# Kernel optimization log

Measured on AMD Instinct MI355X. Metric: run time of the kernel, lower is better.

The kernel has to match this reference:

```python
import jax, jax.numpy as jnp
import numpy as np
from functools import partial

B, EMB, H, V, T = 128, 512, 1024, 8192, 100
START_VALUE = 0


def setup_inputs() -> dict:
    key = jax.random.key(0)
    ks = jax.random.split(key, 8)
    s = 0.05
    return {
        "x": jax.random.normal(ks[0], (B, H), jnp.float32),
        "emb_table": jax.random.normal(ks[1], (V, EMB), jnp.float32) * s,
        "w_ih": jax.random.normal(ks[2], (3 * H, EMB), jnp.float32) * s,
        "w_hh": jax.random.normal(ks[3], (3 * H, H), jnp.float32) * s,
        "b_ih": jax.random.normal(ks[4], (3 * H,), jnp.float32) * s,
        "b_hh": jax.random.normal(ks[5], (3 * H,), jnp.float32) * s,
        "cls_w": jax.random.normal(ks[6], (V, H), jnp.float32) * s,
        "cls_b": jax.random.normal(ks[7], (V,), jnp.float32) * s,
    }


def _gru_cell(e, h, w_ih, w_hh, b_ih, b_hh):
    # PyTorch GRU cell math. e: [B,EMB], h: [B,H]
    gi = e @ w_ih.T + b_ih  # [B, 3H]
    gh = h @ w_hh.T + b_hh  # [B, 3H]
    i_r, i_z, i_n = jnp.split(gi, 3, axis=1)
    h_r, h_z, h_n = jnp.split(gh, 3, axis=1)
    r = jax.nn.sigmoid(i_r + h_r)
    z = jax.nn.sigmoid(i_z + h_z)
    n = jnp.tanh(i_n + r * h_n)
    return (1.0 - z) * n + z * h


def reference(x, emb_table, w_ih, w_hh, b_ih, b_hh, cls_w, cls_b):
    # start distribution: log_softmax of one-hot at START_VALUE
    start_val = jax.nn.log_softmax(
        jnp.zeros((V,), x.dtype).at[START_VALUE].set(1.0), axis=0
    )
    prev0 = jnp.broadcast_to(start_val, (B, V))

    def step(carry, _):
        h, prev_logp = carry
        idx = jnp.argmax(prev_logp, axis=1)          # [B]
        e = emb_table[idx]                           # [B, EMB]
        h_new = _gru_cell(e, h, w_ih, w_hh, b_ih, b_hh)
        logp = jax.nn.log_softmax(h_new @ cls_w.T + cls_b, axis=1)  # [B, V]
        return (h_new, logp), logp

    _, outs = jax.lax.scan(step, (x, prev0), None, length=T - 1)
    outs = jnp.transpose(outs, (1, 0, 2))            # [B, T-1, V]
    return jnp.concatenate([prev0[:, None, :], outs], axis=1)  # [B, T, V]
```

## Files before the change

kernel.cpp:

```cpp
#include <hip/hip_runtime.h>
#include <stdint.h>


#define Bb   128
#define EMBd 512
#define Hd   1024
#define Vd   8192
#define Td   100
#define HPB  524288

typedef __attribute__((ext_vector_type(8))) _Float16 half8;
typedef __attribute__((ext_vector_type(4))) float f32x4;
typedef unsigned long long ull;

#define LOSCALE 2048.0f
#define LOINV   (1.0f/2048.0f)

#define WAITV(N) do { asm volatile("s_waitcnt vmcnt(" #N ")" ::: "memory"); \
                      __builtin_amdgcn_sched_barrier(0); } while (0)
#define WAITL    do { asm volatile("s_waitcnt lgkmcnt(0)" ::: "memory");    \
                      __builtin_amdgcn_sched_barrier(0); } while (0)

__device__ __forceinline__ uint32_t fkey(float f) {
  uint32_t u = __float_as_uint(f);
  return (u & 0x80000000u) ? ~u : (u | 0x80000000u);
}
__device__ __forceinline__ ull umax64(ull a, ull b) { return a > b ? a : b; }

__device__ __forceinline__ void dma16(const void* g, void* l) {
  __builtin_amdgcn_global_load_lds((const uint32_t*)g, (uint32_t*)l, 16, 0, 0);
}
__device__ __forceinline__ void st16sc(void* p, half8 v) {
  f32x4 d = *(f32x4*)&v;
  asm volatile("global_store_dwordx4 %0, %1, off sc0 sc1"
               :: "v"(p), "v"(d) : "memory");
}
__device__ __forceinline__ ull sysld64(const ull* p) {
  return __hip_atomic_load((ull*)p, __ATOMIC_RELAXED, __HIP_MEMORY_SCOPE_SYSTEM);
}

__device__ __forceinline__ void cvt8(const float4 v0, const float4 v1,
                                     half8& hh, half8& ll) {
  float vv[8] = {v0.x, v0.y, v0.z, v0.w, v1.x, v1.y, v1.z, v1.w};
#pragma unroll
  for (int i = 0; i < 8; ++i) {
    _Float16 h = (_Float16)vv[i];
    hh[i] = h;
    ll[i] = (_Float16)((vv[i] - (float)h) * LOSCALE);
  }
}

__global__ void k_init(const float* __restrict__ x, float* __restrict__ hbuf0,
                       ull* __restrict__ amax, char* __restrict__ hpre0,
                       uint32_t* __restrict__ bar) {
  int tid = blockIdx.x * 256 + threadIdx.x;
  if (tid < Bb * Hd) hbuf0[tid] = x[tid];
  if (tid < Td * Bb) amax[tid] = (tid < Bb) ? 0xFFFFFFFFull : 0ull;
  if (tid >= 16384 && tid < 16384 + 256) bar[tid - 16384] = 0;
  if (tid < 16384) {
    int b = tid & 127, sc = tid >> 7;
    int st = sc >> 2, c = sc & 3;
    const float* src = x + b * Hd + st * 32 + c * 8;
    float4 v0 = *(const float4*)src, v1 = *(const float4*)(src + 4);
    half8 hh, ll; cvt8(v0, v1, hh, ll);
    char* hp = hpre0 + st * 16384 + b * 128;
    *(half8*)(hp + ((c       ^ (b & 7))) * 16) = hh;
    *(half8*)(hp + (((c + 4) ^ (b & 7))) * 16) = ll;
  }
}

__global__ void k_prep_emb(const float* __restrict__ emb, char* __restrict__ embp) {
  int t = blockIdx.x * 256 + threadIdx.x;
  int row = t >> 6, rem = t & 63, st = rem >> 2, c = rem & 3;
  const float* src = emb + (size_t)row * EMBd + st * 32 + c * 8;
  float4 v0 = *(const float4*)src, v1 = *(const float4*)(src + 4);
  half8 hh, ll; cvt8(v0, v1, hh, ll);
  char* d = embp + (size_t)row * 2048 + st * 128;
  *(half8*)(d + c * 16) = hh;
  *(half8*)(d + (c + 4) * 16) = ll;
}

__global__ void k_prep_w(const float* __restrict__ w_ih, const float* __restrict__ w_hh,
                         char* __restrict__ wpre) {
  int bi = blockIdx.x;
  int st = bi % 12, t2 = bi / 12, q = t2 & 3, cg = t2 >> 2;
  int t = threadIdx.x; if (t >= 192) return;
  int r = t >> 2, c = t & 3;
  int g = r >> 4, bn = r & 15;
  int k0 = q * 384 + st * 32 + c * 8;
  const float* src = (k0 < 512)
    ? (w_ih + (size_t)(g * 1024 + cg * 16 + bn) * EMBd + k0)
    : (w_hh + (size_t)(g * 1024 + cg * 16 + bn) * Hd + (k0 - 512));
  float4 v0 = *(const float4*)src, v1 = *(const float4*)(src + 4);
  half8 hh, ll; cvt8(v0, v1, hh, ll);
  char* d = wpre + (size_t)bi * 6144 + r * 128;
  *(half8*)(d + ((c       ^ (r & 7))) * 16) = hh;
  *(half8*)(d + (((c + 4) ^ (r & 7))) * 16) = ll;
}

__global__ void k_prep_cls(const float* __restrict__ cls_w, char* __restrict__ clsp) {
  int b = blockIdx.x;
  int ct = b >> 5, st = b & 31;
  int t = threadIdx.x;
  int r = t >> 2, c = t & 3;
  const float* src = cls_w + (size_t)(ct * 64 + r) * Hd + st * 32 + c * 8;
  float4 v0 = *(const float4*)src, v1 = *(const float4*)(src + 4);
  half8 hh, ll; cvt8(v0, v1, hh, ll);
  char* d = clsp + (size_t)b * 8192 + r * 128;
  *(half8*)(d + ((c       ^ (r & 7))) * 16) = hh;
  *(half8*)(d + (((c + 4) ^ (r & 7))) * 16) = ll;
}

__global__ __launch_bounds__(256, 2) void k_prep_gi(
    const char* __restrict__ embp, const char* __restrict__ wpre,
    const float* __restrict__ b_ih, float* __restrict__ gi)
{
  const int cg = blockIdx.x, vh = blockIdx.y;
  const int tid = threadIdx.x, lane = tid & 63, w = tid >> 6;
  const int C = cg * 16;
  __shared__ __align__(16) char pA[4 * 8192];
  __shared__ __align__(16) char pB[4 * 6144];

  f32x4 accH[3], accL[3];
#pragma unroll
  for (int g = 0; g < 3; ++g) {
    accH[g] = (f32x4){0.f, 0.f, 0.f, 0.f};
    accL[g] = (f32x4){0.f, 0.f, 0.f, 0.f};
  }

  const int rr = lane >> 3, cc = lane & 7;
  const char* abase = embp + (size_t)(vh * 64 + w * 16 + rr) * 2048 + ((cc ^ rr) * 16);

  auto issue = [&](int st) {
    char* da = pA + (st & 3) * 8192 + w * 2048;
    const char* s0 = abase + st * 128;
    dma16(s0, da);
    dma16(s0 + 8 * 2048, da + 1024);
    const int wq = st / 12, wst = st - wq * 12;
    const char* sb = wpre + (size_t)((cg * 4 + wq) * 12 + wst) * 6144 + w * 1536 + lane * 16;
    char* db = pB + (st & 3) * 6144 + w * 1536;
    dma16(sb, db);
    if (lane < 32) dma16(sb + 1024, db + 1024);
  };

  const int l15 = lane & 15, qd = lane >> 4, r7 = l15 & 7;
  const int offAH = (w * 16 + l15) * 128 + ((qd)     ^ r7) * 16;
  const int offAL = (w * 16 + l15) * 128 + ((qd + 4) ^ r7) * 16;

  issue(0); issue(1); issue(2);
  WAITV(8);
  __builtin_amdgcn_s_barrier();

  for (int st = 0; st < 16; ++st) {
    const int bf = st & 3;
    half8 aH = *(half8*)&pA[bf * 8192 + offAH];
    half8 aL = *(half8*)&pA[bf * 8192 + offAL];
    if (st + 3 < 16) issue(st + 3);
#pragma unroll
    for (int g = 0; g < 3; ++g) {
      half8 bH = *(half8*)&pB[bf * 6144 + (g * 16 + l15) * 128 + ((qd)     ^ r7) * 16];
      half8 bL = *(half8*)&pB[bf * 6144 + (g * 16 + l15) * 128 + ((qd + 4) ^ r7) * 16];
      accH[g] = __builtin_amdgcn_mfma_f32_16x16x32_f16(aH, bH, accH[g], 0, 0, 0);
      accL[g] = __builtin_amdgcn_mfma_f32_16x16x32_f16(aH, bL, accL[g], 0, 0, 0);
      accL[g] = __builtin_amdgcn_mfma_f32_16x16x32_f16(aL, bH, accL[g], 0, 0, 0);
    }
    if (st < 15) {
      if (st <= 12)      { WAITV(8); }
      else if (st == 13) { WAITV(4); }
      else               { WAITV(0); }
      WAITL;
      __builtin_amdgcn_s_barrier();
    }
  }

  const int v0 = vh * 64 + w * 16 + qd * 4;
#pragma unroll
  for (int g = 0; g < 3; ++g) {
    float bi = b_ih[g * 1024 + C + l15];
#pragma unroll
    for (int i = 0; i < 4; ++i) {
      float val = accH[g][i] + accL[g][i] * LOINV + bi;
      gi[(size_t)(v0 + i) * 3072 + g * 1024 + C + l15] = val;
    }
  }
}

__device__ __forceinline__ void relbar(uint32_t* __restrict__ bar, int wg, uint32_t gen) {
  __syncthreads();
  if (threadIdx.x == 0) {
    const int g = wg & 7;
    uint32_t old = __hip_atomic_fetch_add(&bar[g * 16], 1u, __ATOMIC_RELAXED,
                                          __HIP_MEMORY_SCOPE_SYSTEM);
    if (old + 1u == gen * 32u)
      __hip_atomic_fetch_add(&bar[128], 1u, __ATOMIC_RELAXED,
                             __HIP_MEMORY_SCOPE_SYSTEM);
    while (__hip_atomic_load(&bar[128], __ATOMIC_RELAXED,
                             __HIP_MEMORY_SCOPE_SYSTEM) < gen * 8u)
      __builtin_amdgcn_s_sleep(4);
  }
  __syncthreads();
}

__global__ __launch_bounds__(256) void k_loop(
    const char* __restrict__ wpre, const char* __restrict__ clsp,
    const float* __restrict__ gi,
    const float* __restrict__ b_hh, const float* __restrict__ cls_b,
    float* __restrict__ hbuf, char* __restrict__ hpre,
    ull* __restrict__ amax, float* __restrict__ out,
    uint32_t* __restrict__ bar)
{
  const int wg = blockIdx.x;
  const int tid = threadIdx.x, lane = tid & 63, w = tid >> 6;
  __shared__ __align__(16) char smem[81920];

  if (tid == 0)
    (void)__hip_atomic_load(&bar[160], __ATOMIC_ACQUIRE, __HIP_MEMORY_SCOPE_AGENT);
  __syncthreads();

  const int l15 = lane & 15, qd = lane >> 4, r7 = l15 & 7;

  const int cg = wg & 63, rh = (wg >> 6) & 1;
  const int C = cg * 16;
  const int ct = wg & 127, rt0 = wg >> 7;
  const int r0c = rt0 * 64, c0c = ct * 64;
  const char* c_bsrc = clsp + (size_t)ct * 262144 + w * 2048 + lane * 16;

  const int offA_H = (w * 16 + l15) * 128 + ((qd)     ^ r7) * 16;
  const int offA_L = (w * 16 + l15) * 128 + ((qd + 4) ^ r7) * 16;

  uint32_t gen = 0;

  for (int s = 1; s < Td; ++s) {
    const int pPrev = (s - 1) & 1, pCur = s & 1;
    const char* hpre_rd = hpre + (size_t)(s - 1) * HPB;
    char*       hpre_wr = hpre + (size_t)s * HPB;

    if (wg < 128) {
      const ull* amax_prev = amax + (size_t)(s - 1) * Bb;
      const char* hsrc = hpre_rd + rh * 8192 + w * 2048 + lane * 16;
      char* gA = smem;
      char* gB = smem + 32768;

      f32x4 accH[3], accL[3];
#pragma unroll
      for (int g = 0; g < 3; ++g) {
        accH[g] = (f32x4){0.f, 0.f, 0.f, 0.f};
        accL[g] = (f32x4){0.f, 0.f, 0.f, 0.f};
      }

      auto issue = [&](int st) {
        char* da = gA + (st & 3) * 8192 + w * 2048;
        const char* sa = hsrc + st * 16384;
        dma16(sa, da);
        dma16(sa + 1024, da + 1024);
        const int k0 = 512 + st * 32;
        const int wq = (k0 >= 1152) ? 3 : (k0 >= 768 ? 2 : 1);
        const int wst = (k0 - wq * 384) >> 5;
        const char* sb = wpre + (size_t)((cg * 4 + wq) * 12 + wst) * 6144 + w * 1536 + lane * 16;
        char* db = gB + (st & 3) * 6144 + w * 1536;
        dma16(sb, db);
        if (lane < 32) dma16(sb + 1024, db + 1024);
      };

      issue(0); issue(1); issue(2);
      WAITV(8);
      __builtin_amdgcn_s_barrier();

      for (int st = 0; st < 32; ++st) {
        const int bf = st & 3;
        half8 aH = *(half8*)&gA[bf * 8192 + offA_H];
        half8 aL = *(half8*)&gA[bf * 8192 + offA_L];
        if (st + 3 < 32) issue(st + 3);
#pragma unroll
        for (int g = 0; g < 3; ++g) {
          half8 bH = *(half8*)&gB[bf * 6144 + (g * 16 + l15) * 128 + ((qd)     ^ r7) * 16];
          half8 bL = *(half8*)&gB[bf * 6144 + (g * 16 + l15) * 128 + ((qd + 4) ^ r7) * 16];
          accH[g] = __builtin_amdgcn_mfma_f32_16x16x32_f16(aH, bH, accH[g], 0, 0, 0);
          accL[g] = __builtin_amdgcn_mfma_f32_16x16x32_f16(aH, bL, accL[g], 0, 0, 0);
          accL[g] = __builtin_amdgcn_mfma_f32_16x16x32_f16(aL, bH, accL[g], 0, 0, 0);
        }
        if (st < 31) {
          if (st <= 28)      { WAITV(8); }
          else if (st == 29) { WAITV(4); }
          else               { WAITV(0); }
          WAITL;
          __builtin_amdgcn_s_barrier();
        }
      }

      const int j = C + l15;
      const float bh0 = b_hh[j], bh1 = b_hh[1024 + j], bh2 = b_hh[2048 + j];
      const float* hprev_f = hbuf + (size_t)pPrev * Bb * Hd;
      float* hnew_f = hbuf + (size_t)pCur * Bb * Hd;
      float outs[4];
#pragma unroll
      for (int i = 0; i < 4; ++i) {
        const int ri = rh * 64 + w * 16 + qd * 4 + i;
        const uint32_t idx = (~(uint32_t)sysld64(&amax_prev[ri])) & 8191u;
        const float* gp = gi + (size_t)idx * 3072 + j;
        float i_r = gp[0], i_z = gp[1024], i_n = gp[2048];
        float h_r = accH[0][i] + accL[0][i] * LOINV + bh0;
        float h_z = accH[1][i] + accL[1][i] * LOINV + bh1;
        float h_n = accH[2][i] + accL[2][i] * LOINV + bh2;
        float rr2 = 1.f / (1.f + expf(-(i_r + h_r)));
        float zz = 1.f / (1.f + expf(-(i_z + h_z)));
        float nn = tanhf(i_n + rr2 * h_n);
        float o = (1.f - zz) * nn + zz * hprev_f[ri * Hd + j];
        hnew_f[ri * Hd + j] = o;
        outs[i] = o;
      }
      __syncthreads();
      float* sT = (float*)smem;
#pragma unroll
      for (int i = 0; i < 4; ++i)
        sT[(w * 16 + qd * 4 + i) * 16 + l15] = outs[i];
      __syncthreads();
      if (tid < 128) {
        const int row = tid >> 1, half = tid & 1;
        const int b = rh * 64 + row;
        const float* srcp = sT + row * 16 + half * 8;
        half8 hh, ll;
#pragma unroll
        for (int e = 0; e < 8; ++e) {
          float o = srcp[e];
          _Float16 oh = (_Float16)o;
          hh[e] = oh;
          ll[e] = (_Float16)((o - (float)oh) * LOSCALE);
        }
        const int stp = C >> 5;
        const int chb = ((C & 31) >> 3) + half;
        char* hp = hpre_wr + stp * 16384 + b * 128;
        st16sc(hp + ((chb       ^ (b & 7))) * 16, hh);
        st16sc(hp + (((chb + 4) ^ (b & 7))) * 16, ll);
      }
    }

    ++gen; relbar(bar, wg, gen);

    {
      const char* asrc = hpre_wr + rt0 * 8192 + w * 2048 + lane * 16;
      char* cA = smem;
      char* cB = smem + 32768;

      f32x4 accH[4], accL[4];
#pragma unroll
      for (int i = 0; i < 4; ++i) {
        accH[i] = (f32x4){0.f, 0.f, 0.f, 0.f};
        accL[i] = (f32x4){0.f, 0.f, 0.f, 0.f};
      }

      auto issue = [&](int st) {
        char* da = cA + (st & 3) * 8192 + w * 2048;
        const char* sa = asrc + st * 16384;
        dma16(sa, da);
        dma16(sa + 1024, da + 1024);
        char* db = cB + (st & 3) * 8192 + w * 2048;
        const char* sb = c_bsrc + st * 8192;
        dma16(sb, db);
        dma16(sb + 1024, db + 1024);
      };

      issue(0); issue(1); issue(2);
      WAITV(8);
      __builtin_amdgcn_s_barrier();

      for (int st = 0; st < 32; ++st) {
        const int bf = st & 3;
        half8 aH = *(half8*)&cA[bf * 8192 + offA_H];
        half8 aL = *(half8*)&cA[bf * 8192 + offA_L];
        if (st + 3 < 32) issue(st + 3);
#pragma unroll
        for (int cf = 0; cf < 4; ++cf) {
          half8 bH = *(half8*)&cB[bf * 8192 + (cf * 16 + l15) * 128 + ((qd)     ^ r7) * 16];
          half8 bL = *(half8*)&cB[bf * 8192 + (cf * 16 + l15) * 128 + ((qd + 4) ^ r7) * 16];
          accH[cf] = __builtin_amdgcn_mfma_f32_16x16x32_f16(aH, bH, accH[cf], 0, 0, 0);
          accL[cf] = __builtin_amdgcn_mfma_f32_16x16x32_f16(aH, bL, accL[cf], 0, 0, 0);
          accL[cf] = __builtin_amdgcn_mfma_f32_16x16x32_f16(aL, bH, accL[cf], 0, 0, 0);
        }
        if (st < 31) {
          if (st <= 28)      { WAITV(8); }
          else if (st == 29) { WAITV(4); }
          else               { WAITV(0); }
          WAITL;
          __builtin_amdgcn_s_barrier();
        }
      }

      float bsv[4];
#pragma unroll
      for (int cf = 0; cf < 4; ++cf) bsv[cf] = cls_b[c0c + cf * 16 + l15];
#pragma unroll
      for (int i = 0; i < 4; ++i) {
        const int brow = r0c + w * 16 + qd * 4 + i;
        float* orow = out + ((size_t)brow * Td + s) * Vd;
        ull best = 0ull;
#pragma unroll
        for (int cf = 0; cf < 4; ++cf) {
          const int v = c0c + cf * 16 + l15;
          float val = accH[cf][i] + accL[cf][i] * LOINV + bsv[cf];
          __builtin_nontemporal_store(val, &orow[v]);
          best = umax64(best, ((ull)fkey(val) << 32) | (uint32_t)(~(uint32_t)v));
        }
        best = umax64(best, __shfl_xor(best, 1));
        best = umax64(best, __shfl_xor(best, 2));
        best = umax64(best, __shfl_xor(best, 4));
        best = umax64(best, __shfl_xor(best, 8));
        if (l15 == 0) atomicMax(&amax[(size_t)s * Bb + brow], best);
      }
    }

    ++gen; relbar(bar, wg, gen);
  }
}

__global__ void k_softmax(float* __restrict__ out,
                          const ull* __restrict__ amax) {
  int blk = blockIdx.x;
  int t = blk % Td, b = blk / Td;
  int tid = threadIdx.x;
  float* row = out + ((size_t)b * Td + t) * Vd;
  if (t == 0) {
    float lse0 = logf(expf(1.0f) + (float)(Vd - 1));
    for (int i = tid; i < Vd; i += 256) row[i] = ((i == 0) ? 1.0f : 0.0f) - lse0;
    return;
  }
  ull key = amax[t * Bb + b];
  uint32_t ku = (uint32_t)(key >> 32);
  uint32_t u = (ku & 0x80000000u) ? (ku & 0x7fffffffu) : ~ku;
  float m = __uint_as_float(u);
  float x[32];
  float ssum = 0.f;
#pragma unroll
  for (int i = 0; i < 32; ++i) {
    x[i] = row[tid + i * 256];
    ssum += expf(x[i] - m);
  }
  ssum += __shfl_xor(ssum, 1);
  ssum += __shfl_xor(ssum, 2);
  ssum += __shfl_xor(ssum, 4);
  ssum += __shfl_xor(ssum, 8);
  ssum += __shfl_xor(ssum, 16);
  ssum += __shfl_xor(ssum, 32);
  __shared__ float wsum[4];
  if ((tid & 63) == 0) wsum[tid >> 6] = ssum;
  __syncthreads();
  float lse = m + logf(wsum[0] + wsum[1] + wsum[2] + wsum[3]);
#pragma unroll
  for (int i = 0; i < 32; ++i) row[tid + i * 256] = x[i] - lse;
}

extern "C" void kernel_launch(void* const* d_in, const int* in_sizes, int n_in,
                              void* d_out, int out_size, void* d_ws, size_t ws_size,
                              hipStream_t stream) {
  const float* x     = (const float*)d_in[0];
  const float* emb   = (const float*)d_in[1];
  const float* w_ih  = (const float*)d_in[2];
  const float* w_hh  = (const float*)d_in[3];
  const float* b_ih  = (const float*)d_in[4];
  const float* b_hh  = (const float*)d_in[5];
  const float* cls_w = (const float*)d_in[6];
  const float* cls_b = (const float*)d_in[7];
  float* out = (float*)d_out;

  char* ws = (char*)d_ws;
  size_t o = 0;
  ull*      amax = (ull*)(ws + o);      o += (size_t)Td * Bb * 8;
  uint32_t* bar  = (uint32_t*)(ws + o); o += 1024;
  float*    hbuf = (float*)(ws + o);    o += (size_t)2 * Bb * Hd * 4;
  char*     hpre = ws + o;              o += (size_t)Td * HPB;
  char*     embp = ws + o;              o += (size_t)Vd * 2048;
  char*     wpre = ws + o;              o += (size_t)3072 * 6144;
  char*     clsp = ws + o;              o += (size_t)128 * 32 * 8192;
  float*    gi   = (float*)(ws + o);    o += (size_t)Vd * 3072 * 4;

  k_init<<<512, 256, 0, stream>>>(x, hbuf, amax, hpre, bar);
  k_prep_emb<<<2048, 256, 0, stream>>>(emb, embp);
  k_prep_w<<<3072, 256, 0, stream>>>(w_ih, w_hh, wpre);
  k_prep_cls<<<4096, 256, 0, stream>>>(cls_w, clsp);
  k_prep_gi<<<dim3(64, 128), 256, 0, stream>>>(embp, wpre, b_ih, gi);

  k_loop<<<256, 256, 0, stream>>>(wpre, clsp, gi, b_hh, cls_b,
                                  hbuf, hpre, amax, out, bar);

  k_softmax<<<12800, 256, 0, stream>>>(out, amax);
}
```

Measured before the change: 4.325 ms.

## Split GRU and classifier into dedicated workgroups with flag-based producer/consumer sync

Replaces the two global barriers per timestep with per-step readiness counters. The first 128 workgroups do the GRU step and publish an hReady counter. The remaining workgroups compute the classifier, each covering two column tiles, and publish per-step completion counts. The GRU's hidden-state matmul for step s can now overlap the classifier of step s-1, and it waits for the argmax only before the gate update. In exchange, each classifier workgroup does twice the work with a larger LDS footprint, and correctness depends on the grid size and the counter initialization matching.

Measured after the change: 4.366 ms. No clear change (+0.9%).

```diff
diff --git a/kernel.cpp b/kernel.cpp
--- a/kernel.cpp
+++ b/kernel.cpp
@@ -38,6 +38,15 @@
 __device__ __forceinline__ ull sysld64(const ull* p) {
   return __hip_atomic_load((ull*)p, __ATOMIC_RELAXED, __HIP_MEMORY_SCOPE_SYSTEM);
 }
+__device__ __forceinline__ uint32_t ld32sys(uint32_t* p) {
+  return __hip_atomic_load(p, __ATOMIC_RELAXED, __HIP_MEMORY_SCOPE_SYSTEM);
+}
+__device__ __forceinline__ void st32sys(uint32_t* p, uint32_t v) {
+  __hip_atomic_store(p, v, __ATOMIC_RELAXED, __HIP_MEMORY_SCOPE_SYSTEM);
+}
+__device__ __forceinline__ uint32_t add32sys(uint32_t* p, uint32_t v) {
+  return __hip_atomic_fetch_add(p, v, __ATOMIC_RELAXED, __HIP_MEMORY_SCOPE_SYSTEM);
+}
 
 __device__ __forceinline__ void cvt8(const float4 v0, const float4 v1,
                                      half8& hh, half8& ll) {
@@ -56,7 +65,8 @@
   int tid = blockIdx.x * 256 + threadIdx.x;
   if (tid < Bb * Hd) hbuf0[tid] = x[tid];
   if (tid < Td * Bb) amax[tid] = (tid < Bb) ? 0xFFFFFFFFull : 0ull;
-  if (tid >= 16384 && tid < 16384 + 256) bar[tid - 16384] = 0;
+  if (tid >= 16384 && tid < 16640)
+    bar[tid - 16384] = (tid - 16384 == 8) ? 128u : 0u;
   if (tid < 16384) {
     int b = tid & 127, sc = tid >> 7;
     int st = sc >> 2, c = sc & 3;
@@ -185,22 +195,6 @@
   }
 }
 
-__device__ __forceinline__ void relbar(uint32_t* __restrict__ bar, int wg, uint32_t gen) {
-  __syncthreads();
-  if (threadIdx.x == 0) {
-    const int g = wg & 7;
-    uint32_t old = __hip_atomic_fetch_add(&bar[g * 16], 1u, __ATOMIC_RELAXED,
-                                          __HIP_MEMORY_SCOPE_SYSTEM);
-    if (old + 1u == gen * 32u)
-      __hip_atomic_fetch_add(&bar[128], 1u, __ATOMIC_RELAXED,
-                             __HIP_MEMORY_SCOPE_SYSTEM);
-    while (__hip_atomic_load(&bar[128], __ATOMIC_RELAXED,
-                             __HIP_MEMORY_SCOPE_SYSTEM) < gen * 8u)
-      __builtin_amdgcn_s_sleep(4);
-  }
-  __syncthreads();
-}
-
 __global__ __launch_bounds__(256) void k_loop(
     const char* __restrict__ wpre, const char* __restrict__ clsp,
     const float* __restrict__ gi,
@@ -211,35 +205,32 @@
 {
   const int wg = blockIdx.x;
   const int tid = threadIdx.x, lane = tid & 63, w = tid >> 6;
-  __shared__ __align__(16) char smem[81920];
+  __shared__ __align__(16) char smem[98304];
 
   if (tid == 0)
-    (void)__hip_atomic_load(&bar[160], __ATOMIC_ACQUIRE, __HIP_MEMORY_SCOPE_AGENT);
+    (void)__hip_atomic_load(&bar[200], __ATOMIC_ACQUIRE, __HIP_MEMORY_SCOPE_AGENT);
   __syncthreads();
 
+  uint32_t* gCnt   = &bar[0];
+  uint32_t* hReady = &bar[1];
+  uint32_t* aCnt   = &bar[8];
+
   const int l15 = lane & 15, qd = lane >> 4, r7 = l15 & 7;
-
-  const int cg = wg & 63, rh = (wg >> 6) & 1;
-  const int C = cg * 16;
-  const int ct = wg & 127, rt0 = wg >> 7;
-  const int r0c = rt0 * 64, c0c = ct * 64;
-  const char* c_bsrc = clsp + (size_t)ct * 262144 + w * 2048 + lane * 16;
-
   const int offA_H = (w * 16 + l15) * 128 + ((qd)     ^ r7) * 16;
   const int offA_L = (w * 16 + l15) * 128 + ((qd + 4) ^ r7) * 16;
 
-  uint32_t gen = 0;
-
-  for (int s = 1; s < Td; ++s) {
-    const int pPrev = (s - 1) & 1, pCur = s & 1;
-    const char* hpre_rd = hpre + (size_t)(s - 1) * HPB;
-    char*       hpre_wr = hpre + (size_t)s * HPB;
-
-    if (wg < 128) {
-      const ull* amax_prev = amax + (size_t)(s - 1) * Bb;
-      const char* hsrc = hpre_rd + rh * 8192 + w * 2048 + lane * 16;
-      char* gA = smem;
-      char* gB = smem + 32768;
+  if (wg < 128) {
+    const int cg = wg & 63, rh = wg >> 6;
+    const int C = cg * 16;
+    char* gA = smem;
+    char* gB = smem + 32768;
+
+    for (int s = 1; s < Td; ++s) {
+      if (tid == 0)
+        while (ld32sys(hReady) < (uint32_t)(s - 1)) __builtin_amdgcn_s_sleep(2);
+      __syncthreads();
+
+      const char* hsrc = hpre + (size_t)(s - 1) * HPB + rh * 8192 + w * 2048 + lane * 16;
 
       f32x4 accH[3], accL[3];
 #pragma unroll
@@ -288,10 +279,15 @@
         }
       }
 
+      if (tid == 0)
+        while (ld32sys(&aCnt[s - 1]) < 128u) __builtin_amdgcn_s_sleep(2);
+      __syncthreads();
+
       const int j = C + l15;
       const float bh0 = b_hh[j], bh1 = b_hh[1024 + j], bh2 = b_hh[2048 + j];
-      const float* hprev_f = hbuf + (size_t)pPrev * Bb * Hd;
-      float* hnew_f = hbuf + (size_t)pCur * Bb * Hd;
+      const float* hprev_f = hbuf + (size_t)((s - 1) & 1) * Bb * Hd;
+      float* hnew_f = hbuf + (size_t)(s & 1) * Bb * Hd;
+      const ull* amax_prev = amax + (size_t)(s - 1) * Bb;
       float outs[4];
 #pragma unroll
       for (int i = 0; i < 4; ++i) {
@@ -329,22 +325,37 @@
         }
         const int stp = C >> 5;
         const int chb = ((C & 31) >> 3) + half;
-        char* hp = hpre_wr + stp * 16384 + b * 128;
+        char* hp = hpre + (size_t)s * HPB + stp * 16384 + b * 128;
         st16sc(hp + ((chb       ^ (b & 7))) * 16, hh);
         st16sc(hp + (((chb + 4) ^ (b & 7))) * 16, ll);
       }
+      WAITV(0);
+      __syncthreads();
+      if (tid == 0) {
+        uint32_t old = add32sys(gCnt, 1u);
+        if (old + 1u == 128u * (uint32_t)s)
+          st32sys(hReady, (uint32_t)s);
+      }
     }
-
-    ++gen; relbar(bar, wg, gen);
-
-    {
-      const char* asrc = hpre_wr + rt0 * 8192 + w * 2048 + lane * 16;
-      char* cA = smem;
-      char* cB = smem + 32768;
-
-      f32x4 accH[4], accL[4];
-#pragma unroll
-      for (int i = 0; i < 4; ++i) {
+  } else {
+    const int wgC = wg - 128;
+    const int ct2 = wgC & 63, rt0 = wgC >> 6;
+    const int r0c = rt0 * 64;
+    char* cA = smem;
+    char* cB = smem + 32768;
+    const char* bb0 = clsp + (size_t)(2 * ct2)     * 262144 + w * 2048 + lane * 16;
+    const char* bb1 = clsp + (size_t)(2 * ct2 + 1) * 262144 + w * 2048 + lane * 16;
+
+    for (int s = 1; s < Td; ++s) {
+      if (tid == 0)
+        while (ld32sys(hReady) < (uint32_t)s) __builtin_amdgcn_s_sleep(2);
+      __syncthreads();
+
+      const char* asrc = hpre + (size_t)s * HPB + rt0 * 8192 + w * 2048 + lane * 16;
+
+      f32x4 accH[8], accL[8];
+#pragma unroll
+      for (int i = 0; i < 8; ++i) {
         accH[i] = (f32x4){0.f, 0.f, 0.f, 0.f};
         accL[i] = (f32x4){0.f, 0.f, 0.f, 0.f};
       }
@@ -354,14 +365,17 @@
         const char* sa = asrc + st * 16384;
         dma16(sa, da);
         dma16(sa + 1024, da + 1024);
-        char* db = cB + (st & 3) * 8192 + w * 2048;
-        const char* sb = c_bsrc + st * 8192;
-        dma16(sb, db);
-        dma16(sb + 1024, db + 1024);
+        char* db = cB + (st & 3) * 16384 + w * 2048;
+        const char* s0 = bb0 + st * 8192;
+        dma16(s0, db);
+        dma16(s0 + 1024, db + 1024);
+        const char* s1 = bb1 + st * 8192;
+        dma16(s1, db + 8192);
+        dma16(s1 + 1024, db + 8192 + 1024);
       };
 
       issue(0); issue(1); issue(2);
-      WAITV(8);
+      WAITV(12);
       __builtin_amdgcn_s_barrier();
 
       for (int st = 0; st < 32; ++st) {
@@ -370,33 +384,35 @@
         half8 aL = *(half8*)&cA[bf * 8192 + offA_L];
         if (st + 3 < 32) issue(st + 3);
 #pragma unroll
-        for (int cf = 0; cf < 4; ++cf) {
-          half8 bH = *(half8*)&cB[bf * 8192 + (cf * 16 + l15) * 128 + ((qd)     ^ r7) * 16];
-          half8 bL = *(half8*)&cB[bf * 8192 + (cf * 16 + l15) * 128 + ((qd + 4) ^ r7) * 16];
+        for (int cf = 0; cf < 8; ++cf) {
+          const int bo = bf * 16384 + (cf >> 2) * 8192 + ((cf & 3) * 16 + l15) * 128;
+          half8 bH = *(half8*)&cB[bo + ((qd)     ^ r7) * 16];
+          half8 bL = *(half8*)&cB[bo + ((qd + 4) ^ r7) * 16];
           accH[cf] = __builtin_amdgcn_mfma_f32_16x16x32_f16(aH, bH, accH[cf], 0, 0, 0);
           accL[cf] = __builtin_amdgcn_mfma_f32_16x16x32_f16(aH, bL, accL[cf], 0, 0, 0);
           accL[cf] = __builtin_amdgcn_mfma_f32_16x16x32_f16(aL, bH, accL[cf], 0, 0, 0);
         }
         if (st < 31) {
-          if (st <= 28)      { WAITV(8); }
-          else if (st == 29) { WAITV(4); }
+          if (st <= 28)      { WAITV(12); }
+          else if (st == 29) { WAITV(6); }
           else               { WAITV(0); }
           WAITL;
           __builtin_amdgcn_s_barrier();
         }
       }
 
-      float bsv[4];
-#pragma unroll
-      for (int cf = 0; cf < 4; ++cf) bsv[cf] = cls_b[c0c + cf * 16 + l15];
+      float bsv[8];
+#pragma unroll
+      for (int cf = 0; cf < 8; ++cf)
+        bsv[cf] = cls_b[(2 * ct2 + (cf >> 2)) * 64 + (cf & 3) * 16 + l15];
 #pragma unroll
       for (int i = 0; i < 4; ++i) {
         const int brow = r0c + w * 16 + qd * 4 + i;
         float* orow = out + ((size_t)brow * Td + s) * Vd;
         ull best = 0ull;
 #pragma unroll
-        for (int cf = 0; cf < 4; ++cf) {
-          const int v = c0c + cf * 16 + l15;
+        for (int cf = 0; cf < 8; ++cf) {
+          const int v = (2 * ct2 + (cf >> 2)) * 64 + (cf & 3) * 16 + l15;
           float val = accH[cf][i] + accL[cf][i] * LOINV + bsv[cf];
           __builtin_nontemporal_store(val, &orow[v]);
           best = umax64(best, ((ull)fkey(val) << 32) | (uint32_t)(~(uint32_t)v));
@@ -407,9 +423,10 @@
         best = umax64(best, __shfl_xor(best, 8));
         if (l15 == 0) atomicMax(&amax[(size_t)s * Bb + brow], best);
       }
+      WAITV(0);
+      __syncthreads();
+      if (tid == 0) add32sys(&aCnt[s], 1u);
     }
-
-    ++gen; relbar(bar, wg, gen);
   }
 }
 
```
